# Kernel tuning notes

Hardware: AMD Instinct MI355X
Metric: run time of the kernel (lower is better)

Reference implementation:

```python
import jax, jax.numpy as jnp
import numpy as np

D_MODEL = 1024
N_HEADS = 16
D_K = D_MODEL // N_HEADS
FF_DIM = 4096
EPS = 1e-6
NEG = -1.0e9


def _layernorm(x, g, b):
    # torch: a_2 * (x - mean) / (std + eps) + b_2, std is unbiased (ddof=1)
    mean = jnp.mean(x, axis=-1, keepdims=True)
    std = jnp.std(x, axis=-1, keepdims=True, ddof=1)
    return g * (x - mean) / (std + EPS) + b


def setup_inputs() -> dict:
    key = jax.random.key(0)
    ks = jax.random.split(key, 8)
    s = 0.02
    x = jax.random.normal(ks[0], (2, 2048, D_MODEL), dtype=jnp.float32)
    mask = jnp.ones((2, 1, 1, 2048), dtype=jnp.int32)
    return {
        "x": x,
        "mask": mask,
        "wq": jax.random.normal(ks[1], (D_MODEL, D_MODEL), jnp.float32) * s,
        "wk": jax.random.normal(ks[2], (D_MODEL, D_MODEL), jnp.float32) * s,
        "wv": jax.random.normal(ks[3], (D_MODEL, D_MODEL), jnp.float32) * s,
        "wo": jax.random.normal(ks[4], (D_MODEL, D_MODEL), jnp.float32) * s,
        "bq": jnp.zeros((D_MODEL,), jnp.float32),
        "bk": jnp.zeros((D_MODEL,), jnp.float32),
        "bv": jnp.zeros((D_MODEL,), jnp.float32),
        "bo": jnp.zeros((D_MODEL,), jnp.float32),
        "w1": jax.random.normal(ks[5], (D_MODEL, FF_DIM), jnp.float32) * s,
        "b1": jnp.zeros((FF_DIM,), jnp.float32),
        "w2": jax.random.normal(ks[6], (FF_DIM, D_MODEL), jnp.float32) * s,
        "b2": jnp.zeros((D_MODEL,), jnp.float32),
        "ln1_g": jnp.ones((D_MODEL,), jnp.float32),
        "ln1_b": jnp.zeros((D_MODEL,), jnp.float32),
        "ln2_g": jnp.ones((D_MODEL,), jnp.float32),
        "ln2_b": jnp.zeros((D_MODEL,), jnp.float32),
    }


def reference(x, mask, wq, wk, wv, wo, bq, bk, bv, bo, w1, b1, w2, b2,
              ln1_g, ln1_b, ln2_g, ln2_b):
    B, S, _ = x.shape
    # --- sublayer 1: pre-norm self-attention with residual ---
    h = _layernorm(x, ln1_g, ln1_b)
    q = (h @ wq + bq).reshape(B, S, N_HEADS, D_K).transpose(0, 2, 1, 3)
    k = (h @ wk + bk).reshape(B, S, N_HEADS, D_K).transpose(0, 2, 1, 3)
    v = (h @ wv + bv).reshape(B, S, N_HEADS, D_K).transpose(0, 2, 1, 3)
    scores = jnp.einsum('bhqd,bhkd->bhqk', q, k) / np.sqrt(D_K).astype(np.float32)
    scores = jnp.where(mask == 0, NEG, scores)
    attn = jax.nn.softmax(scores, axis=-1)
    ctx = jnp.einsum('bhqk,bhkd->bhqd', attn, v)
    ctx = ctx.transpose(0, 2, 1, 3).reshape(B, S, D_MODEL)
    x = x + (ctx @ wo + bo)
    # --- sublayer 2: pre-norm FFN with residual ---
    h2 = _layernorm(x, ln2_g, ln2_b)
    ff = jax.nn.relu(h2 @ w1 + b1) @ w2 + b2
    return x + ff
```

## Files before the change

kernel.cpp:

```cpp
#include <hip/hip_runtime.h>

typedef unsigned short u16;
typedef __attribute__((ext_vector_type(8))) short bf16x8;
typedef __attribute__((ext_vector_type(4))) float f32x4;

__device__ __forceinline__ u16 f2bf(float f) {
  union { float f; unsigned int u; } x;
  x.f = f;
  unsigned int r = x.u + 0x7fffu + ((x.u >> 16) & 1u);
  return (u16)(r >> 16);
}

__device__ __forceinline__ float bf2f(u16 v) {
  union { unsigned int u; float f; } x;
  x.u = ((unsigned int)v) << 16;
  return x.f;
}

__device__ __forceinline__ void async16(const u16* g, u16* l) {
  __builtin_amdgcn_global_load_lds((const __attribute__((address_space(1))) void*)g,
                                   (__attribute__((address_space(3))) void*)l, 16, 0, 0);
}

__device__ __forceinline__ void stage128x64(const u16* __restrict__ src, long row0, int k0,
                                            int ld, u16* lds, int wave, int lane) {
#pragma unroll
  for (int r = 0; r < 4; ++r) {
    int s = r * 256 + wave * 64 + lane;
    int row = s >> 3;
    int c = (s & 7) ^ (row & 7);
    async16(src + (row0 + row) * (long)ld + k0 + c * 8, lds + (r * 256 + wave * 64) * 8);
  }
}

__device__ __forceinline__ void stage64x128(const u16* __restrict__ src, int col0, int ld,
                                            u16* lds, int wave, int lane) {
#pragma unroll
  for (int r = 0; r < 4; ++r) {
    int s = r * 256 + wave * 64 + lane;
    int row = s >> 4;
    int c = (s & 15) ^ (row & 15);
    async16(src + (long)row * ld + col0 + c * 8, lds + (r * 256 + wave * 64) * 8);
  }
}

__global__ __launch_bounds__(256) void transpose_cvt(const float* __restrict__ src,
                                                     u16* __restrict__ dst, int R, int C) {
  __shared__ float tile[32][33];
  int c0 = blockIdx.x * 32, r0 = blockIdx.y * 32;
  int tx = threadIdx.x & 31, ty = threadIdx.x >> 5;
#pragma unroll
  for (int i = 0; i < 32; i += 8)
    tile[ty + i][tx] = src[(long)(r0 + ty + i) * C + c0 + tx];
  __syncthreads();
#pragma unroll
  for (int i = 0; i < 32; i += 8)
    dst[(long)(c0 + ty + i) * R + r0 + tx] = f2bf(tile[tx][ty + i]);
}

__global__ __launch_bounds__(256) void transpose_cvt4(const float* __restrict__ s0,
                                                      const float* __restrict__ s1,
                                                      const float* __restrict__ s2,
                                                      const float* __restrict__ s3,
                                                      u16* __restrict__ dst) {
  __shared__ float tile[32][33];
  const float* src = blockIdx.z == 0 ? s0 : (blockIdx.z == 1 ? s1 : (blockIdx.z == 2 ? s2 : s3));
  u16* d = dst + (long)blockIdx.z * 1024 * 1024;
  int c0 = blockIdx.x * 32, r0 = blockIdx.y * 32;
  int tx = threadIdx.x & 31, ty = threadIdx.x >> 5;
#pragma unroll
  for (int i = 0; i < 32; i += 8)
    tile[ty + i][tx] = src[(long)(r0 + ty + i) * 1024 + c0 + tx];
  __syncthreads();
#pragma unroll
  for (int i = 0; i < 32; i += 8)
    d[(long)(c0 + ty + i) * 1024 + r0 + tx] = f2bf(tile[tx][ty + i]);
}

__device__ __forceinline__ void ln_core(float4 v, const float* g, const float* b, int t,
                                        u16* outrow) {
  float s = v.x + v.y + v.z + v.w;
  float ss = v.x * v.x + v.y * v.y + v.z * v.z + v.w * v.w;
#pragma unroll
  for (int off = 32; off; off >>= 1) {
    s += __shfl_xor(s, off);
    ss += __shfl_xor(ss, off);
  }
  __shared__ float red[8];
  int wave = t >> 6, lane = t & 63;
  if (lane == 0) { red[wave] = s; red[wave + 4] = ss; }
  __syncthreads();
  float tot = red[0] + red[1] + red[2] + red[3];
  float tots = red[4] + red[5] + red[6] + red[7];
  float mean = tot * (1.0f / 1024.0f);
  float var = (tots - 1024.0f * mean * mean) * (1.0f / 1023.0f);
  var = fmaxf(var, 0.0f);
  float inv = 1.0f / (sqrtf(var) + 1e-6f);
  float4 gv = ((const float4*)g)[t];
  float4 bv = ((const float4*)b)[t];
  union { unsigned long long u64; u16 h[4]; } o;
  o.h[0] = f2bf(gv.x * (v.x - mean) * inv + bv.x);
  o.h[1] = f2bf(gv.y * (v.y - mean) * inv + bv.y);
  o.h[2] = f2bf(gv.z * (v.z - mean) * inv + bv.z);
  o.h[3] = f2bf(gv.w * (v.w - mean) * inv + bv.w);
  *(unsigned long long*)(outrow + t * 4) = o.u64;
}

__global__ __launch_bounds__(256) void layernorm_rows(const float* __restrict__ x,
                                                      const float* __restrict__ g,
                                                      const float* __restrict__ b,
                                                      u16* __restrict__ out) {
  int row = blockIdx.x, t = threadIdx.x;
  float4 v = ((const float4*)(x + (long)row * 1024))[t];
  ln_core(v, g, b, t, out + (long)row * 1024);
}

__global__ __launch_bounds__(256) void ln_fuse(const float* __restrict__ x,
                                               const float* __restrict__ bres,
                                               const u16* __restrict__ p0,
                                               const u16* __restrict__ p1,
                                               const float* __restrict__ g,
                                               const float* __restrict__ b,
                                               float* __restrict__ yout,
                                               u16* __restrict__ hout) {
  int row = blockIdx.x, t = threadIdx.x;
  long base = (long)row * 1024;
  float4 xv = ((const float4*)(x + base))[t];
  float4 bo = ((const float4*)bres)[t];
  ushort4 a = ((const ushort4*)(p0 + base))[t];
  ushort4 c = ((const ushort4*)(p1 + base))[t];
  float4 y;
  y.x = xv.x + bo.x + bf2f(a.x) + bf2f(c.x);
  y.y = xv.y + bo.y + bf2f(a.y) + bf2f(c.y);
  y.z = xv.z + bo.z + bf2f(a.z) + bf2f(c.z);
  y.w = xv.w + bo.w + bf2f(a.w) + bf2f(c.w);
  ((float4*)(yout + base))[t] = y;
  ln_core(y, g, b, t, hout + base);
}

__global__ __launch_bounds__(256) void final_add(float* __restrict__ out,
                                                 const float* __restrict__ b2,
                                                 const u16* __restrict__ p0,
                                                 const u16* __restrict__ p1) {
  int row = blockIdx.x, t = threadIdx.x;
  long base = (long)row * 1024;
  float4 o = ((float4*)(out + base))[t];
  float4 bb = ((const float4*)b2)[t];
  ushort4 a = ((const ushort4*)(p0 + base))[t];
  ushort4 c = ((const ushort4*)(p1 + base))[t];
  o.x += bb.x + bf2f(a.x) + bf2f(c.x);
  o.y += bb.y + bf2f(a.y) + bf2f(c.y);
  o.z += bb.z + bf2f(a.z) + bf2f(c.z);
  o.w += bb.w + bf2f(a.w) + bf2f(c.w);
  ((float4*)(out + base))[t] = o;
}

template <int MODE>
__global__ __launch_bounds__(256) void gemm_bt(const u16* __restrict__ A,
                                               const u16* __restrict__ Bt, int M, int N, int K,
                                               void* __restrict__ outp,
                                               const float* __restrict__ bias0,
                                               const float* __restrict__ bias1,
                                               const float* __restrict__ bias2,
                                               u16* __restrict__ q_out, u16* __restrict__ k_out,
                                               u16* __restrict__ v_out) {
  __shared__ __align__(16) u16 lds[17408];
  u16* ldsA = lds;
  u16* ldsB = lds + 8192;
  const int tid = threadIdx.x;
  const int wave = tid >> 6, lane = tid & 63;
  const int lane16 = lane & 15, quad = lane >> 4;
  const int wm = (wave >> 1) * 64, wn = (wave & 1) * 64;
  const long m0 = (long)blockIdx.y * 128;
  const long n0 = (long)blockIdx.x * 128;
  const int kLen = K / gridDim.z;
  const int kBeg = blockIdx.z * kLen;

  const f32x4 fzero = {0.f, 0.f, 0.f, 0.f};
  f32x4 acc[4][4];
#pragma unroll
  for (int i = 0; i < 4; ++i)
#pragma unroll
    for (int j = 0; j < 4; ++j) acc[i][j] = fzero;

  for (int k0 = kBeg; k0 < kBeg + kLen; k0 += 64) {
    stage128x64(A, m0, k0, K, ldsA, wave, lane);
    stage128x64(Bt, n0, k0, K, ldsB, wave, lane);
    __syncthreads();
#pragma unroll
    for (int kk = 0; kk < 2; ++kk) {
      bf16x8 af[4], bfr[4];
#pragma unroll
      for (int i = 0; i < 4; ++i) {
        int row = wm + i * 16 + lane16;
        int c = (kk * 4 + quad) ^ (row & 7);
        af[i] = *(const bf16x8*)(ldsA + row * 64 + c * 8);
      }
#pragma unroll
      for (int j = 0; j < 4; ++j) {
        int row = wn + j * 16 + lane16;
        int c = (kk * 4 + quad) ^ (row & 7);
        bfr[j] = *(const bf16x8*)(ldsB + row * 64 + c * 8);
      }
#pragma unroll
      for (int i = 0; i < 4; ++i)
#pragma unroll
        for (int j = 0; j < 4; ++j)
          acc[i][j] = __builtin_amdgcn_mfma_f32_16x16x32_bf16(af[i], bfr[j], acc[i][j], 0, 0, 0);
    }
    __syncthreads();
  }

  if (MODE == 0 && (int)(n0 >> 10) == 2) {
#pragma unroll
    for (int j = 0; j < 4; ++j) {
      int lcol = wn + j * 16 + lane16;
      float bvj = bias2[(int)(n0 - 2048) + lcol];
#pragma unroll
      for (int i = 0; i < 4; ++i)
#pragma unroll
        for (int r = 0; r < 4; ++r) {
          int lrow = wm + i * 16 + quad * 4 + r;
          lds[lcol * 136 + lrow] = f2bf(acc[i][j][r] + bvj);
        }
    }
    __syncthreads();
    int lcol = tid >> 1, seg = tid & 1;
    int cc = (int)(n0 - 2048) + lcol;
    int head = cc >> 6, d = cc & 63;
    int bI = (int)(m0 >> 11), s0 = (int)(m0 & 2047);
    u16* dst = v_out + ((long)(bI * 16 + head) * 64 + d) * 2048 + s0 + seg * 64;
    const u16* s = lds + lcol * 136 + seg * 64;
#pragma unroll
    for (int c2 = 0; c2 < 8; ++c2) ((uint4*)dst)[c2] = ((const uint4*)s)[c2];
    return;
  }

#pragma unroll
  for (int j = 0; j < 4; ++j) {
    int col = (int)n0 + wn + j * 16 + lane16;
#pragma unroll
    for (int i = 0; i < 4; ++i) {
#pragma unroll
      for (int r = 0; r < 4; ++r) {
        int row = (int)m0 + wm + i * 16 + quad * 4 + r;
        float val = acc[i][j][r];
        if (MODE == 0) {
          int which = col >> 10, cc = col & 1023;
          float vv = val + (which == 0 ? bias0[cc] : bias1[cc]);
          int bb = row >> 11, sS = row & 2047, head = cc >> 6, d = cc & 63;
          long bh = (long)bb * 16 + head;
          if (which == 0) {
            q_out[(bh * 2048 + sS) * 64 + d] = f2bf(vv * 0.18033688f);
          } else {
            k_out[(bh * 2048 + sS) * 64 + d] = f2bf(vv);
          }
        } else if (MODE == 1) {
          ((u16*)outp)[((long)blockIdx.z * M + row) * (long)N + col] = f2bf(val);
        } else if (MODE == 2) {
          ((u16*)outp)[(long)row * N + col] = f2bf(fmaxf(val + bias0[col], 0.0f));
        }
      }
    }
  }
}

#define FA_C0 28.854239f
__global__ __launch_bounds__(256) void flash_attn(const u16* __restrict__ q,
                                                  const u16* __restrict__ k,
                                                  const u16* __restrict__ v,
                                                  const int* __restrict__ mask,
                                                  u16* __restrict__ ctx) {
  const int bh = blockIdx.y;
  const int b = bh >> 4, h = bh & 15;
  const int q0 = blockIdx.x * 64;
  const int tid = threadIdx.x;
  const int wave = tid >> 6, lane = tid & 63;
  const int lane16 = lane & 15, quad = lane >> 4;

  const u16* qp = q + (long)bh * 2048 * 64;
  const u16* kp = k + (long)bh * 2048 * 64;
  const u16* vp = v + (long)bh * 64 * 2048;
  const int* mp = mask + b * 2048;

  __shared__ u16 ldsK[128 * 64];
  __shared__ u16 ldsVT[64 * 128];
  __shared__ float ldsMask[128];
  u16* myP = ldsK + wave * (16 * 128);

  bf16x8 qf[2];
  {
    const long qrow = q0 + wave * 16 + lane16;
    qf[0] = *(const bf16x8*)(qp + qrow * 64 + quad * 8);
    qf[1] = *(const bf16x8*)(qp + qrow * 64 + 32 + quad * 8);
  }

  const f32x4 fzero = {0.f, 0.f, 0.f, 0.f};
  float l_i[4] = {0.f, 0.f, 0.f, 0.f};
  f32x4 o_acc[4];
#pragma unroll
  for (int j = 0; j < 4; ++j) o_acc[j] = fzero;

  for (int kt = 0; kt < 2048; kt += 128) {
    stage128x64(kp, kt, 0, 64, ldsK, wave, lane);
    stage64x128(vp, kt, 2048, ldsVT, wave, lane);
    if (tid < 128) ldsMask[tid] = ((mp[kt + tid] == 0) ? -1.0e9f : 0.0f) - FA_C0;
    __syncthreads();

    f32x4 s_acc[8];
#pragma unroll
    for (int j = 0; j < 8; ++j) {
      float c0 = ldsMask[j * 16 + lane16];
      s_acc[j] = f32x4{c0, c0, c0, c0};
#pragma unroll
      for (int kk = 0; kk < 2; ++kk) {
        int row = j * 16 + lane16;
        int c = (kk * 4 + quad) ^ (row & 7);
        bf16x8 kf = *(const bf16x8*)(ldsK + row * 64 + c * 8);
        s_acc[j] = __builtin_amdgcn_mfma_f32_16x16x32_bf16(qf[kk], kf, s_acc[j], 0, 0, 0);
      }
    }
    __syncthreads();

#pragma unroll
    for (int j = 0; j < 8; ++j) {
#pragma unroll
      for (int r = 0; r < 4; ++r) {
        float p = __builtin_exp2f(s_acc[j][r]);
        l_i[r] += p;
        int prow = quad * 4 + r;
        int pcol = j * 16 + lane16;
        int cswz = (pcol >> 3) ^ (prow & 7);
        myP[prow * 128 + cswz * 8 + (pcol & 7)] = f2bf(p);
      }
    }
#pragma unroll
    for (int kk = 0; kk < 4; ++kk) {
      int c = (kk * 4 + quad) ^ (lane16 & 7);
      bf16x8 pf = *(const bf16x8*)(myP + lane16 * 128 + c * 8);
#pragma unroll
      for (int jj = 0; jj < 4; ++jj) {
        int row = jj * 16 + lane16;
        int cv = (kk * 4 + quad) ^ (row & 15);
        bf16x8 vf = *(const bf16x8*)(ldsVT + row * 128 + cv * 8);
        o_acc[jj] = __builtin_amdgcn_mfma_f32_16x16x32_bf16(pf, vf, o_acc[jj], 0, 0, 0);
      }
    }
    __syncthreads();
  }

#pragma unroll
  for (int r = 0; r < 4; ++r) {
#pragma unroll
    for (int off = 1; off < 16; off <<= 1) l_i[r] += __shfl_xor(l_i[r], off);
    l_i[r] = 1.0f / l_i[r];
  }
#pragma unroll
  for (int jj = 0; jj < 4; ++jj) {
#pragma unroll
    for (int r = 0; r < 4; ++r) {
      int sg = q0 + wave * 16 + quad * 4 + r;
      int d = jj * 16 + lane16;
      float val = o_acc[jj][r] * l_i[r];
      ctx[((long)b * 2048 + sg) * 1024 + h * 64 + d] = f2bf(val);
    }
  }
}

extern "C" void kernel_launch(void* const* d_in, const int* in_sizes, int n_in, void* d_out,
                              int out_size, void* d_ws, size_t ws_size, hipStream_t stream) {
  (void)in_sizes; (void)n_in; (void)out_size; (void)ws_size;
  const float* x  = (const float*)d_in[0];
  const int* mask = (const int*)d_in[1];
  const float* wq = (const float*)d_in[2];
  const float* wk = (const float*)d_in[3];
  const float* wv = (const float*)d_in[4];
  const float* wo = (const float*)d_in[5];
  const float* bq = (const float*)d_in[6];
  const float* bk = (const float*)d_in[7];
  const float* bv = (const float*)d_in[8];
  const float* bo = (const float*)d_in[9];
  const float* w1 = (const float*)d_in[10];
  const float* b1 = (const float*)d_in[11];
  const float* w2 = (const float*)d_in[12];
  const float* b2 = (const float*)d_in[13];
  const float* ln1_g = (const float*)d_in[14];
  const float* ln1_b = (const float*)d_in[15];
  const float* ln2_g = (const float*)d_in[16];
  const float* ln2_b = (const float*)d_in[17];
  float* out = (float*)d_out;

  u16* ws = (u16*)d_ws;
  u16* wqkvT = ws;
  u16* woT = wqkvT + 3072 * 1024;
  u16* w1T = woT + 1024 * 1024;
  u16* w2T = w1T + 4096 * 1024;
  u16* h   = w2T + 4096 * 1024;
  u16* qb  = h + 4096 * 1024;
  u16* kb  = qb + 4096 * 1024;
  u16* vb  = kb + 4096 * 1024;
  u16* ctx = vb + 4096 * 1024;
  u16* ffh = qb;
  u16* f2p = ws;

  transpose_cvt4<<<dim3(32, 32, 4), 256, 0, stream>>>(wq, wk, wv, wo, wqkvT);
  transpose_cvt<<<dim3(128, 32), 256, 0, stream>>>(w1, w1T, 1024, 4096);
  transpose_cvt<<<dim3(32, 128), 256, 0, stream>>>(w2, w2T, 4096, 1024);

  layernorm_rows<<<4096, 256, 0, stream>>>(x, ln1_g, ln1_b, h);

  gemm_bt<0><<<dim3(24, 32), 256, 0, stream>>>(h, wqkvT, 4096, 3072, 1024, nullptr, bq, bk, bv,
                                               qb, kb, vb);

  flash_attn<<<dim3(32, 32), 256, 0, stream>>>(qb, kb, vb, mask, ctx);

  gemm_bt<1><<<dim3(8, 32, 2), 256, 0, stream>>>(ctx, woT, 4096, 1024, 1024, qb, nullptr,
                                                 nullptr, nullptr, nullptr, nullptr, nullptr);

  ln_fuse<<<4096, 256, 0, stream>>>(x, bo, qb, kb, ln2_g, ln2_b, out, h);

  gemm_bt<2><<<dim3(32, 32), 256, 0, stream>>>(h, w1T, 4096, 4096, 1024, ffh, b1, nullptr,
                                               nullptr, nullptr, nullptr, nullptr);

  gemm_bt<1><<<dim3(8, 32, 2), 256, 0, stream>>>(ffh, w2T, 4096, 1024, 4096, f2p, nullptr,
                                                 nullptr, nullptr, nullptr, nullptr, nullptr);

  final_add<<<4096, 256, 0, stream>>>(out, b2, f2p, f2p + 4096 * 1024);
}
```

Measured before the change: 388.7 us.

## Deepen split-K for output projections and streamline flash-attention softmax path

The Wo GEMM now uses 4-way split-K and the W2 GEMM uses an uneven 3-way split-K, so each launches more blocks. The partial results go to separate dead workspace buffers and are summed in ln_fuse and final_add. Flash attention swaps the MFMA operand order so each lane holds key scores for a single query. This allows packed bf16 stores of P via perm and a cheaper row-sum reduction. It also adds a ballot-based all-valid mask flag that skips the per-element mask loads. The trade-off is more partial-sum memory traffic in the elementwise kernels and more aliasing of workspace buffers.

```diff
diff --git a/kernel.cpp b/kernel.cpp
--- a/kernel.cpp
+++ b/kernel.cpp
@@ -1,6 +1,7 @@
 #include <hip/hip_runtime.h>
 
 typedef unsigned short u16;
+typedef unsigned int u32;
 typedef __attribute__((ext_vector_type(8))) short bf16x8;
 typedef __attribute__((ext_vector_type(4))) float f32x4;
 
@@ -15,6 +16,10 @@
   union { unsigned int u; float f; } x;
   x.u = ((unsigned int)v) << 16;
   return x.f;
+}
+
+__device__ __forceinline__ u32 fbits(float f) {
+  union { float f; u32 u; } x; x.f = f; return x.u;
 }
 
 __device__ __forceinline__ void async16(const u16* g, u16* l) {
@@ -119,6 +124,8 @@
                                                const float* __restrict__ bres,
                                                const u16* __restrict__ p0,
                                                const u16* __restrict__ p1,
+                                               const u16* __restrict__ p2,
+                                               const u16* __restrict__ p3,
                                                const float* __restrict__ g,
                                                const float* __restrict__ b,
                                                float* __restrict__ yout,
@@ -129,11 +136,13 @@
   float4 bo = ((const float4*)bres)[t];
   ushort4 a = ((const ushort4*)(p0 + base))[t];
   ushort4 c = ((const ushort4*)(p1 + base))[t];
+  ushort4 d = ((const ushort4*)(p2 + base))[t];
+  ushort4 e = ((const ushort4*)(p3 + base))[t];
   float4 y;
-  y.x = xv.x + bo.x + bf2f(a.x) + bf2f(c.x);
-  y.y = xv.y + bo.y + bf2f(a.y) + bf2f(c.y);
-  y.z = xv.z + bo.z + bf2f(a.z) + bf2f(c.z);
-  y.w = xv.w + bo.w + bf2f(a.w) + bf2f(c.w);
+  y.x = xv.x + bo.x + bf2f(a.x) + bf2f(c.x) + bf2f(d.x) + bf2f(e.x);
+  y.y = xv.y + bo.y + bf2f(a.y) + bf2f(c.y) + bf2f(d.y) + bf2f(e.y);
+  y.z = xv.z + bo.z + bf2f(a.z) + bf2f(c.z) + bf2f(d.z) + bf2f(e.z);
+  y.w = xv.w + bo.w + bf2f(a.w) + bf2f(c.w) + bf2f(d.w) + bf2f(e.w);
   ((float4*)(yout + base))[t] = y;
   ln_core(y, g, b, t, hout + base);
 }
@@ -141,17 +150,19 @@
 __global__ __launch_bounds__(256) void final_add(float* __restrict__ out,
                                                  const float* __restrict__ b2,
                                                  const u16* __restrict__ p0,
-                                                 const u16* __restrict__ p1) {
+                                                 const u16* __restrict__ p1,
+                                                 const u16* __restrict__ p2) {
   int row = blockIdx.x, t = threadIdx.x;
   long base = (long)row * 1024;
   float4 o = ((float4*)(out + base))[t];
   float4 bb = ((const float4*)b2)[t];
   ushort4 a = ((const ushort4*)(p0 + base))[t];
   ushort4 c = ((const ushort4*)(p1 + base))[t];
-  o.x += bb.x + bf2f(a.x) + bf2f(c.x);
-  o.y += bb.y + bf2f(a.y) + bf2f(c.y);
-  o.z += bb.z + bf2f(a.z) + bf2f(c.z);
-  o.w += bb.w + bf2f(a.w) + bf2f(c.w);
+  ushort4 d = ((const ushort4*)(p2 + base))[t];
+  o.x += bb.x + bf2f(a.x) + bf2f(c.x) + bf2f(d.x);
+  o.y += bb.y + bf2f(a.y) + bf2f(c.y) + bf2f(d.y);
+  o.z += bb.z + bf2f(a.z) + bf2f(c.z) + bf2f(d.z);
+  o.w += bb.w + bf2f(a.w) + bf2f(c.w) + bf2f(d.w);
   ((float4*)(out + base))[t] = o;
 }
 
@@ -173,8 +184,14 @@
   const int wm = (wave >> 1) * 64, wn = (wave & 1) * 64;
   const long m0 = (long)blockIdx.y * 128;
   const long n0 = (long)blockIdx.x * 128;
-  const int kLen = K / gridDim.z;
-  const int kBeg = blockIdx.z * kLen;
+  int kLen, kBeg;
+  if (gridDim.z == 3) {
+    kLen = (blockIdx.z == 0) ? 1408 : 1344;
+    kBeg = blockIdx.z ? (1408 + (blockIdx.z - 1) * 1344) : 0;
+  } else {
+    kLen = K / gridDim.z;
+    kBeg = blockIdx.z * kLen;
+  }
 
   const f32x4 fzero = {0.f, 0.f, 0.f, 0.f};
   f32x4 acc[4][4];
@@ -234,6 +251,11 @@
 #pragma unroll
     for (int c2 = 0; c2 < 8; ++c2) ((uint4*)dst)[c2] = ((const uint4*)s)[c2];
     return;
+  }
+
+  u16* pp = nullptr;
+  if (MODE == 1) {
+    pp = blockIdx.z == 0 ? (u16*)outp : (blockIdx.z == 1 ? q_out : (blockIdx.z == 2 ? k_out : v_out));
   }
 
 #pragma unroll
@@ -256,7 +278,7 @@
             k_out[(bh * 2048 + sS) * 64 + d] = f2bf(vv);
           }
         } else if (MODE == 1) {
-          ((u16*)outp)[((long)blockIdx.z * M + row) * (long)N + col] = f2bf(val);
+          pp[(long)row * N + col] = f2bf(val);
         } else if (MODE == 2) {
           ((u16*)outp)[(long)row * N + col] = f2bf(fmaxf(val + bias0[col], 0.0f));
         }
@@ -283,10 +305,11 @@
   const u16* vp = v + (long)bh * 64 * 2048;
   const int* mp = mask + b * 2048;
 
-  __shared__ u16 ldsK[128 * 64];
-  __shared__ u16 ldsVT[64 * 128];
-  __shared__ float ldsMask[128];
-  u16* myP = ldsK + wave * (16 * 128);
+  __shared__ __align__(16) u16 ldsK[128 * 64];
+  __shared__ __align__(16) u16 ldsVT[64 * 128];
+  __shared__ __align__(16) float ldsMask[128];
+  __shared__ int ldsFlag[2];
+  u16* myP = ldsK + wave * 2048;
 
   bf16x8 qf[2];
   {
@@ -296,48 +319,58 @@
   }
 
   const f32x4 fzero = {0.f, 0.f, 0.f, 0.f};
-  float l_i[4] = {0.f, 0.f, 0.f, 0.f};
+  const f32x4 cC0 = {-FA_C0, -FA_C0, -FA_C0, -FA_C0};
+  float l_loc = 0.f;
   f32x4 o_acc[4];
 #pragma unroll
   for (int j = 0; j < 4; ++j) o_acc[j] = fzero;
+
+  const int xorm = (lane16 & 7) << 2;
 
   for (int kt = 0; kt < 2048; kt += 128) {
     stage128x64(kp, kt, 0, 64, ldsK, wave, lane);
     stage64x128(vp, kt, 2048, ldsVT, wave, lane);
-    if (tid < 128) ldsMask[tid] = ((mp[kt + tid] == 0) ? -1.0e9f : 0.0f) - FA_C0;
-    __syncthreads();
+    if (tid < 128) {
+      int mv = mp[kt + tid];
+      ldsMask[tid] = ((mv == 0) ? -1.0e9f : 0.0f) - FA_C0;
+      unsigned long long bal = __ballot(mv != 0);
+      if ((tid & 63) == 0) ldsFlag[tid >> 6] = (bal == ~0ull) ? 1 : 0;
+    }
+    __syncthreads();
+    const bool allv = (ldsFlag[0] & ldsFlag[1]) != 0;
 
     f32x4 s_acc[8];
 #pragma unroll
     for (int j = 0; j < 8; ++j) {
-      float c0 = ldsMask[j * 16 + lane16];
-      s_acc[j] = f32x4{c0, c0, c0, c0};
+      f32x4 sa = allv ? cC0 : *(const f32x4*)(ldsMask + j * 16 + quad * 4);
 #pragma unroll
       for (int kk = 0; kk < 2; ++kk) {
         int row = j * 16 + lane16;
         int c = (kk * 4 + quad) ^ (row & 7);
         bf16x8 kf = *(const bf16x8*)(ldsK + row * 64 + c * 8);
-        s_acc[j] = __builtin_amdgcn_mfma_f32_16x16x32_bf16(qf[kk], kf, s_acc[j], 0, 0, 0);
+        sa = __builtin_amdgcn_mfma_f32_16x16x32_bf16(kf, qf[kk], sa, 0, 0, 0);
       }
+      s_acc[j] = sa;
     }
     __syncthreads();
 
 #pragma unroll
     for (int j = 0; j < 8; ++j) {
-#pragma unroll
-      for (int r = 0; r < 4; ++r) {
-        float p = __builtin_exp2f(s_acc[j][r]);
-        l_i[r] += p;
-        int prow = quad * 4 + r;
-        int pcol = j * 16 + lane16;
-        int cswz = (pcol >> 3) ^ (prow & 7);
-        myP[prow * 128 + cswz * 8 + (pcol & 7)] = f2bf(p);
-      }
+      float p0 = __builtin_exp2f(s_acc[j][0]);
+      float p1 = __builtin_exp2f(s_acc[j][1]);
+      float p2 = __builtin_exp2f(s_acc[j][2]);
+      float p3 = __builtin_exp2f(s_acc[j][3]);
+      l_loc += (p0 + p1) + (p2 + p3);
+      u32 lo = __builtin_amdgcn_perm(fbits(p1), fbits(p0), 0x07060302u);
+      u32 hi = __builtin_amdgcn_perm(fbits(p3), fbits(p2), 0x07060302u);
+      int cw = (4 * j + quad) ^ xorm;
+      uint2 pk; pk.x = lo; pk.y = hi;
+      *(uint2*)(myP + lane16 * 128 + cw * 4) = pk;
     }
 #pragma unroll
     for (int kk = 0; kk < 4; ++kk) {
-      int c = (kk * 4 + quad) ^ (lane16 & 7);
-      bf16x8 pf = *(const bf16x8*)(myP + lane16 * 128 + c * 8);
+      int cr = (8 * kk + 2 * quad) ^ xorm;
+      bf16x8 pf = *(const bf16x8*)(myP + lane16 * 128 + cr * 4);
 #pragma unroll
       for (int jj = 0; jj < 4; ++jj) {
         int row = jj * 16 + lane16;
@@ -350,18 +383,19 @@
   }
 
 #pragma unroll
-  for (int r = 0; r < 4; ++r) {
-#pragma unroll
-    for (int off = 1; off < 16; off <<= 1) l_i[r] += __shfl_xor(l_i[r], off);
-    l_i[r] = 1.0f / l_i[r];
-  }
+  for (int off = 16; off < 64; off <<= 1) l_loc += __shfl_xor(l_loc, off);
+  float linv = 1.0f / l_loc;
+  float lr[4];
+#pragma unroll
+  for (int r = 0; r < 4; ++r) lr[r] = __shfl(linv, quad * 4 + r);
+
 #pragma unroll
   for (int jj = 0; jj < 4; ++jj) {
 #pragma unroll
     for (int r = 0; r < 4; ++r) {
       int sg = q0 + wave * 16 + quad * 4 + r;
       int d = jj * 16 + lane16;
-      float val = o_acc[jj][r] * l_i[r];
+      float val = o_acc[jj][r] * lr[r];
       ctx[((long)b * 2048 + sg) * 1024 + h * 64 + d] = f2bf(val);
     }
   }
@@ -401,7 +435,9 @@
   u16* vb  = kb + 4096 * 1024;
   u16* ctx = vb + 4096 * 1024;
   u16* ffh = qb;
-  u16* f2p = ws;
+  u16* f2p0 = ws;
+  u16* f2p1 = w1T;
+  u16* f2p2 = h;
 
   transpose_cvt4<<<dim3(32, 32, 4), 256, 0, stream>>>(wq, wk, wv, wo, wqkvT);
   transpose_cvt<<<dim3(128, 32), 256, 0, stream>>>(w1, w1T, 1024, 4096);
@@ -414,16 +450,16 @@
 
   flash_attn<<<dim3(32, 32), 256, 0, stream>>>(qb, kb, vb, mask, ctx);
 
-  gemm_bt<1><<<dim3(8, 32, 2), 256, 0, stream>>>(ctx, woT, 4096, 1024, 1024, qb, nullptr,
-                                                 nullptr, nullptr, nullptr, nullptr, nullptr);
-
-  ln_fuse<<<4096, 256, 0, stream>>>(x, bo, qb, kb, ln2_g, ln2_b, out, h);
+  gemm_bt<1><<<dim3(8, 32, 4), 256, 0, stream>>>(ctx, woT, 4096, 1024, 1024, h, nullptr,
+                                                 nullptr, nullptr, qb, kb, vb);
+
+  ln_fuse<<<4096, 256, 0, stream>>>(x, bo, h, qb, kb, vb, ln2_g, ln2_b, out, h);
 
   gemm_bt<2><<<dim3(32, 32), 256, 0, stream>>>(h, w1T, 4096, 4096, 1024, ffh, b1, nullptr,
                                                nullptr, nullptr, nullptr, nullptr);
 
-  gemm_bt<1><<<dim3(8, 32, 2), 256, 0, stream>>>(ffh, w2T, 4096, 1024, 4096, f2p, nullptr,
-                                                 nullptr, nullptr, nullptr, nullptr, nullptr);
-
-  final_add<<<4096, 256, 0, stream>>>(out, b2, f2p, f2p + 4096 * 1024);
-}
+  gemm_bt<1><<<dim3(8, 32, 3), 256, 0, stream>>>(ffh, w2T, 4096, 1024, 4096, f2p0, nullptr,
+                                                 nullptr, nullptr, f2p1, f2p2, nullptr);
+
+  final_add<<<4096, 256, 0, stream>>>(out, b2, f2p0, f2p1, f2p2);
+}
```

Result: slower. 408.6 us (+5.1%).

## Process 128 query rows per flash-attention block and skip mask loads when unmasked

Applied to the files above, without the earlier changes.

Each wave now handles two 16-row query groups, so one block covers 128 queries. Each K/V tile staged in LDS is reused twice as much, and the grid is halved. The S computation is transposed (K as the A operand), P is packed into bf16 pairs with perm and written as 8-byte stores, and a ballot check skips per-column mask loads when the whole tile is unmasked. The split-K partial output pointers were also reworked to pick a destination buffer per z-slice. The trade-off is higher register pressure, plus extra LDS for the additional P buffers.

```diff
diff --git a/kernel.cpp b/kernel.cpp
--- a/kernel.cpp
+++ b/kernel.cpp
@@ -1,6 +1,7 @@
 #include <hip/hip_runtime.h>
 
 typedef unsigned short u16;
+typedef unsigned int u32;
 typedef __attribute__((ext_vector_type(8))) short bf16x8;
 typedef __attribute__((ext_vector_type(4))) float f32x4;
 
@@ -15,6 +16,10 @@
   union { unsigned int u; float f; } x;
   x.u = ((unsigned int)v) << 16;
   return x.f;
+}
+
+__device__ __forceinline__ u32 fbits(float f) {
+  union { float f; u32 u; } x; x.f = f; return x.u;
 }
 
 __device__ __forceinline__ void async16(const u16* g, u16* l) {
@@ -236,6 +241,11 @@
     return;
   }
 
+  u16* pp = nullptr;
+  if (MODE == 1) {
+    pp = blockIdx.z == 0 ? (u16*)outp : (blockIdx.z == 1 ? q_out : (blockIdx.z == 2 ? k_out : v_out));
+  }
+
 #pragma unroll
   for (int j = 0; j < 4; ++j) {
     int col = (int)n0 + wn + j * 16 + lane16;
@@ -256,7 +266,7 @@
             k_out[(bh * 2048 + sS) * 64 + d] = f2bf(vv);
           }
         } else if (MODE == 1) {
-          ((u16*)outp)[((long)blockIdx.z * M + row) * (long)N + col] = f2bf(val);
+          pp[(long)row * N + col] = f2bf(val);
         } else if (MODE == 2) {
           ((u16*)outp)[(long)row * N + col] = f2bf(fmaxf(val + bias0[col], 0.0f));
         }
@@ -273,7 +283,7 @@
                                                   u16* __restrict__ ctx) {
   const int bh = blockIdx.y;
   const int b = bh >> 4, h = bh & 15;
-  const int q0 = blockIdx.x * 64;
+  const int q0 = blockIdx.x * 128;
   const int tid = threadIdx.x;
   const int wave = tid >> 6, lane = tid & 63;
   const int lane16 = lane & 15, quad = lane >> 4;
@@ -283,88 +293,117 @@
   const u16* vp = v + (long)bh * 64 * 2048;
   const int* mp = mask + b * 2048;
 
-  __shared__ u16 ldsK[128 * 64];
-  __shared__ u16 ldsVT[64 * 128];
-  __shared__ float ldsMask[128];
-  u16* myP = ldsK + wave * (16 * 128);
-
-  bf16x8 qf[2];
-  {
-    const long qrow = q0 + wave * 16 + lane16;
-    qf[0] = *(const bf16x8*)(qp + qrow * 64 + quad * 8);
-    qf[1] = *(const bf16x8*)(qp + qrow * 64 + 32 + quad * 8);
+  __shared__ __align__(16) u16 ldsK[128 * 64];
+  __shared__ __align__(16) u16 ldsVT[64 * 128];
+  __shared__ __align__(16) u16 ldsP23[2 * 4096];
+  __shared__ __align__(16) float ldsMask[128];
+  __shared__ int ldsFlag[2];
+  u16* myP = (wave < 2) ? (ldsK + wave * 4096) : (ldsP23 + (wave - 2) * 4096);
+
+  bf16x8 qf[2][2];
+#pragma unroll
+  for (int g = 0; g < 2; ++g) {
+    const long qrow = q0 + wave * 32 + g * 16 + lane16;
+    qf[g][0] = *(const bf16x8*)(qp + qrow * 64 + quad * 8);
+    qf[g][1] = *(const bf16x8*)(qp + qrow * 64 + 32 + quad * 8);
   }
 
   const f32x4 fzero = {0.f, 0.f, 0.f, 0.f};
-  float l_i[4] = {0.f, 0.f, 0.f, 0.f};
-  f32x4 o_acc[4];
-#pragma unroll
-  for (int j = 0; j < 4; ++j) o_acc[j] = fzero;
+  const f32x4 cC0 = {-FA_C0, -FA_C0, -FA_C0, -FA_C0};
+  float l_loc[2] = {0.f, 0.f};
+  f32x4 o_acc[2][4];
+#pragma unroll
+  for (int g = 0; g < 2; ++g)
+#pragma unroll
+    for (int j = 0; j < 4; ++j) o_acc[g][j] = fzero;
+
+  const int xorm = (lane16 & 7) << 2;
 
   for (int kt = 0; kt < 2048; kt += 128) {
     stage128x64(kp, kt, 0, 64, ldsK, wave, lane);
     stage64x128(vp, kt, 2048, ldsVT, wave, lane);
-    if (tid < 128) ldsMask[tid] = ((mp[kt + tid] == 0) ? -1.0e9f : 0.0f) - FA_C0;
-    __syncthreads();
-
-    f32x4 s_acc[8];
+    if (tid < 128) {
+      int mv = mp[kt + tid];
+      ldsMask[tid] = ((mv == 0) ? -1.0e9f : 0.0f) - FA_C0;
+      unsigned long long bal = __ballot(mv != 0);
+      if ((tid & 63) == 0) ldsFlag[tid >> 6] = (bal == ~0ull) ? 1 : 0;
+    }
+    __syncthreads();
+    const bool allv = (ldsFlag[0] & ldsFlag[1]) != 0;
+
+    f32x4 s_acc[8][2];
 #pragma unroll
     for (int j = 0; j < 8; ++j) {
-      float c0 = ldsMask[j * 16 + lane16];
-      s_acc[j] = f32x4{c0, c0, c0, c0};
-#pragma unroll
-      for (int kk = 0; kk < 2; ++kk) {
-        int row = j * 16 + lane16;
-        int c = (kk * 4 + quad) ^ (row & 7);
-        bf16x8 kf = *(const bf16x8*)(ldsK + row * 64 + c * 8);
-        s_acc[j] = __builtin_amdgcn_mfma_f32_16x16x32_bf16(qf[kk], kf, s_acc[j], 0, 0, 0);
+      f32x4 ci = allv ? cC0 : *(const f32x4*)(ldsMask + j * 16 + quad * 4);
+      int row = j * 16 + lane16;
+      int c0i = quad ^ (row & 7);
+      int c1i = (4 + quad) ^ (row & 7);
+      bf16x8 kf0 = *(const bf16x8*)(ldsK + row * 64 + c0i * 8);
+      bf16x8 kf1 = *(const bf16x8*)(ldsK + row * 64 + c1i * 8);
+#pragma unroll
+      for (int g = 0; g < 2; ++g) {
+        f32x4 sa = __builtin_amdgcn_mfma_f32_16x16x32_bf16(kf0, qf[g][0], ci, 0, 0, 0);
+        sa = __builtin_amdgcn_mfma_f32_16x16x32_bf16(kf1, qf[g][1], sa, 0, 0, 0);
+        s_acc[j][g] = sa;
       }
     }
     __syncthreads();
 
 #pragma unroll
     for (int j = 0; j < 8; ++j) {
-#pragma unroll
-      for (int r = 0; r < 4; ++r) {
-        float p = __builtin_exp2f(s_acc[j][r]);
-        l_i[r] += p;
-        int prow = quad * 4 + r;
-        int pcol = j * 16 + lane16;
-        int cswz = (pcol >> 3) ^ (prow & 7);
-        myP[prow * 128 + cswz * 8 + (pcol & 7)] = f2bf(p);
+      int cw = (4 * j + quad) ^ xorm;
+#pragma unroll
+      for (int g = 0; g < 2; ++g) {
+        float p0 = __builtin_exp2f(s_acc[j][g][0]);
+        float p1 = __builtin_exp2f(s_acc[j][g][1]);
+        float p2 = __builtin_exp2f(s_acc[j][g][2]);
+        float p3 = __builtin_exp2f(s_acc[j][g][3]);
+        l_loc[g] += (p0 + p1) + (p2 + p3);
+        u32 lo = __builtin_amdgcn_perm(fbits(p1), fbits(p0), 0x07060302u);
+        u32 hi = __builtin_amdgcn_perm(fbits(p3), fbits(p2), 0x07060302u);
+        uint2 pk; pk.x = lo; pk.y = hi;
+        *(uint2*)(myP + (g * 16 + lane16) * 128 + cw * 4) = pk;
       }
     }
 #pragma unroll
     for (int kk = 0; kk < 4; ++kk) {
-      int c = (kk * 4 + quad) ^ (lane16 & 7);
-      bf16x8 pf = *(const bf16x8*)(myP + lane16 * 128 + c * 8);
+      int cr = (8 * kk + 2 * quad) ^ xorm;
+      bf16x8 pf0 = *(const bf16x8*)(myP + lane16 * 128 + cr * 4);
+      bf16x8 pf1 = *(const bf16x8*)(myP + (16 + lane16) * 128 + cr * 4);
 #pragma unroll
       for (int jj = 0; jj < 4; ++jj) {
         int row = jj * 16 + lane16;
         int cv = (kk * 4 + quad) ^ (row & 15);
         bf16x8 vf = *(const bf16x8*)(ldsVT + row * 128 + cv * 8);
-        o_acc[jj] = __builtin_amdgcn_mfma_f32_16x16x32_bf16(pf, vf, o_acc[jj], 0, 0, 0);
-      }
-    }
-    __syncthreads();
-  }
-
-#pragma unroll
-  for (int r = 0; r < 4; ++r) {
-#pragma unroll
-    for (int off = 1; off < 16; off <<= 1) l_i[r] += __shfl_xor(l_i[r], off);
-    l_i[r] = 1.0f / l_i[r];
-  }
-#pragma unroll
-  for (int jj = 0; jj < 4; ++jj) {
-#pragma unroll
-    for (int r = 0; r < 4; ++r) {
-      int sg = q0 + wave * 16 + quad * 4 + r;
-      int d = jj * 16 + lane16;
-      float val = o_acc[jj][r] * l_i[r];
-      ctx[((long)b * 2048 + sg) * 1024 + h * 64 + d] = f2bf(val);
-    }
-  }
+        o_acc[0][jj] = __builtin_amdgcn_mfma_f32_16x16x32_bf16(pf0, vf, o_acc[0][jj], 0, 0, 0);
+        o_acc[1][jj] = __builtin_amdgcn_mfma_f32_16x16x32_bf16(pf1, vf, o_acc[1][jj], 0, 0, 0);
+      }
+    }
+    __syncthreads();
+  }
+
+  float lr[2][4];
+#pragma unroll
+  for (int g = 0; g < 2; ++g) {
+    float l = l_loc[g];
+#pragma unroll
+    for (int off = 16; off < 64; off <<= 1) l += __shfl_xor(l, off);
+    float linv = 1.0f / l;
+#pragma unroll
+    for (int r = 0; r < 4; ++r) lr[g][r] = __shfl(linv, quad * 4 + r);
+  }
+
+#pragma unroll
+  for (int g = 0; g < 2; ++g)
+#pragma unroll
+    for (int jj = 0; jj < 4; ++jj)
+#pragma unroll
+      for (int r = 0; r < 4; ++r) {
+        int sg = q0 + wave * 32 + g * 16 + quad * 4 + r;
+        int d = jj * 16 + lane16;
+        float val = o_acc[g][jj][r] * lr[g][r];
+        ctx[((long)b * 2048 + sg) * 1024 + h * 64 + d] = f2bf(val);
+      }
 }
 
 extern "C" void kernel_launch(void* const* d_in, const int* in_sizes, int n_in, void* d_out,
@@ -401,7 +440,8 @@
   u16* vb  = kb + 4096 * 1024;
   u16* ctx = vb + 4096 * 1024;
   u16* ffh = qb;
-  u16* f2p = ws;
+  u16* f2p0 = ws;
+  u16* f2p1 = w1T;
 
   transpose_cvt4<<<dim3(32, 32, 4), 256, 0, stream>>>(wq, wk, wv, wo, wqkvT);
   transpose_cvt<<<dim3(128, 32), 256, 0, stream>>>(w1, w1T, 1024, 4096);
@@ -412,18 +452,18 @@
   gemm_bt<0><<<dim3(24, 32), 256, 0, stream>>>(h, wqkvT, 4096, 3072, 1024, nullptr, bq, bk, bv,
                                                qb, kb, vb);
 
-  flash_attn<<<dim3(32, 32), 256, 0, stream>>>(qb, kb, vb, mask, ctx);
+  flash_attn<<<dim3(16, 32), 256, 0, stream>>>(qb, kb, vb, mask, ctx);
 
   gemm_bt<1><<<dim3(8, 32, 2), 256, 0, stream>>>(ctx, woT, 4096, 1024, 1024, qb, nullptr,
-                                                 nullptr, nullptr, nullptr, nullptr, nullptr);
+                                                 nullptr, nullptr, kb, nullptr, nullptr);
 
   ln_fuse<<<4096, 256, 0, stream>>>(x, bo, qb, kb, ln2_g, ln2_b, out, h);
 
   gemm_bt<2><<<dim3(32, 32), 256, 0, stream>>>(h, w1T, 4096, 4096, 1024, ffh, b1, nullptr,
                                                nullptr, nullptr, nullptr, nullptr);
 
-  gemm_bt<1><<<dim3(8, 32, 2), 256, 0, stream>>>(ffh, w2T, 4096, 1024, 4096, f2p, nullptr,
-                                                 nullptr, nullptr, nullptr, nullptr, nullptr);
-
-  final_add<<<4096, 256, 0, stream>>>(out, b2, f2p, f2p + 4096 * 1024);
-}
+  gemm_bt<1><<<dim3(8, 32, 2), 256, 0, stream>>>(ffh, w2T, 4096, 1024, 4096, f2p0, nullptr,
+                                                 nullptr, nullptr, f2p1, nullptr, nullptr);
+
+  final_add<<<4096, 256, 0, stream>>>(out, b2, f2p0, f2p1);
+}
```

Measured after the change: 376.7 us. -3.1%, faster.
